# Performance work log

Measured on AMD Instinct MI355X. Metric: run time of the kernel, lower is better.

## Reference

```python
import jax, jax.numpy as jnp
import numpy as np
from jax import lax

C = 173            # EEG channels (independent towers)
L = 400            # samples per channel
POOL_OUT = 10      # AdaptiveMaxPool1d output length (400/10 = 40 exact window)
EPS = 1e-5


def setup_inputs() -> dict:
    key = jax.random.key(0)
    ks = jax.random.split(key, 6)
    B = 64
    x = jax.random.normal(ks[0], (B, C, L), dtype=jnp.float32)
    # per-channel tower 1: Conv1d(1,16,9)  -> grouped kernel [C*16, 1, 9]
    w1 = jax.random.normal(ks[1], (C * 16, 1, 9), dtype=jnp.float32) * 0.2
    b1 = jnp.zeros((C * 16,), jnp.float32)
    g1 = jnp.ones((C * 16,), jnp.float32)
    beta1 = jnp.zeros((C * 16,), jnp.float32)
    m1 = jnp.zeros((C * 16,), jnp.float32)
    v1 = jnp.ones((C * 16,), jnp.float32)
    # per-channel tower 2: Conv1d(16,32,7) -> grouped kernel [C*32, 16, 7]
    w2 = jax.random.normal(ks[2], (C * 32, 16, 7), dtype=jnp.float32) * 0.05
    b2 = jnp.zeros((C * 32,), jnp.float32)
    g2 = jnp.ones((C * 32,), jnp.float32)
    beta2 = jnp.zeros((C * 32,), jnp.float32)
    m2 = jnp.zeros((C * 32,), jnp.float32)
    v2 = jnp.ones((C * 32,), jnp.float32)
    # combiner MLP: Linear(32*C*10, 128) -> ReLU -> Linear(128, 1)
    wc1 = jax.random.normal(ks[3], (128, 32 * C * POOL_OUT), dtype=jnp.float32) * 0.01
    bc1 = jnp.zeros((128,), jnp.float32)
    wc2 = jax.random.normal(ks[4], (1, 128), dtype=jnp.float32) * 0.05
    bc2 = jnp.zeros((1,), jnp.float32)
    return dict(x=x, w1=w1, b1=b1, g1=g1, beta1=beta1, m1=m1, v1=v1,
                w2=w2, b2=b2, g2=g2, beta2=beta2, m2=m2, v2=v2,
                wc1=wc1, bc1=bc1, wc2=wc2, bc2=bc2)


def _bn(y, g, beta, m, v):
    # inference-mode BatchNorm1d over channel axis of [B, CF, L]
    inv = g * lax.rsqrt(v + EPS)
    return y * inv[None, :, None] + (beta - m * inv)[None, :, None]


def reference(x, w1, b1, g1, beta1, m1, v1, w2, b2, g2, beta2, m2, v2, wc1, bc1, wc2, bc2):
    B = x.shape[0]
    dn = ('NCH', 'OIH', 'NCH')
    # tower conv 1: all 173 per-channel Conv1d(1,16,9,pad=4) as one grouped conv
    y = lax.conv_general_dilated(x, w1, (1,), [(4, 4)], dimension_numbers=dn,
                                 feature_group_count=C)           # [B, C*16, 400]
    y = jax.nn.relu(_bn(y + b1[None, :, None], g1, beta1, m1, v1))
    # tower conv 2: Conv1d(16,32,7,pad=3), grouped by channel
    y = lax.conv_general_dilated(y, w2, (1,), [(3, 3)], dimension_numbers=dn,
                                 feature_group_count=C)           # [B, C*32, 400]
    y = jax.nn.relu(_bn(y + b2[None, :, None], g2, beta2, m2, v2))
    # AdaptiveMaxPool1d(10): exact non-overlapping windows of 40
    y = y.reshape(B, C * 32, POOL_OUT, L // POOL_OUT).max(axis=-1)  # [B, C*32, 10]
    # concat of per-channel flattened features == flatten (channel, feat, pos)
    flat = y.reshape(B, C * 32 * POOL_OUT)                          # [B, 55360]
    h = jax.nn.relu(flat @ wc1.T + bc1)
    out = h @ wc2.T + bc2                                           # [B, 1]
    return out
```

## Files before the change

kernel.cpp:

```cpp
#include <hip/hip_runtime.h>

#define C_CH 173
#define L_IN 400
#define EPSV 1e-5f
#define KFEAT 55360

typedef __fp16   fp16x2 __attribute__((ext_vector_type(2)));
typedef _Float16 f16x8  __attribute__((ext_vector_type(8)));
typedef float    f32x4  __attribute__((ext_vector_type(4)));
typedef float    f32x16 __attribute__((ext_vector_type(16)));

#define Y1T_STRIDE_I 9
#define Y1T_ROWS   406

#define SEG_STRIDE 102

#define N1 (173 * 3584)
#define N2 (173 * 512)
#define N3 (173 * 96)

__global__ __launch_bounds__(256) void prep_kernel(
    const float* __restrict__ w1, const float* __restrict__ b1,
    const float* __restrict__ g1, const float* __restrict__ beta1,
    const float* __restrict__ m1, const float* __restrict__ v1,
    const float* __restrict__ w2, const float* __restrict__ b2,
    const float* __restrict__ g2, const float* __restrict__ beta2,
    const float* __restrict__ m2, const float* __restrict__ v2,
    _Float16* __restrict__ w2T_g, _Float16* __restrict__ w1T_g,
    float* __restrict__ sc_g)
{
    const int idx = blockIdx.x * 256 + threadIdx.x;
    if (idx < N1) {
        int c = idx / 3584, r = idx - c * 3584;
        int dt = r >> 9, fg = r & 511;
        int f = fg >> 4, g = fg & 15;
        w2T_g[idx] = (_Float16)w2[c * 3584 + f * 112 + g * 7 + dt];
    } else if (idx < N1 + N2) {
        int j = idx - N1;
        int c = j / 512, r = j - c * 512;
        int g = r >> 5, k = r & 31;
        w1T_g[j] = (k < 9) ? (_Float16)w1[c * 144 + g * 9 + k] : (_Float16)0.0f;
    } else if (idx < N1 + N2 + N3) {
        int j = idx - N1 - N2;
        int c = j / 96, r = j - c * 96;
        float o;
        if (r < 32) {
            int g  = r & 15;
            int cf = c * 16 + g;
            float inv = g1[cf] * rsqrtf(v1[cf] + EPSV);
            o = (r < 16) ? inv : (b1[cf] - m1[cf]) * inv + beta1[cf];
        } else {
            int f  = (r - 32) & 31;
            int cf = c * 32 + f;
            float inv = g2[cf] * rsqrtf(v2[cf] + EPSV);
            o = (r < 64) ? inv : (b2[cf] - m2[cf]) * inv + beta2[cf];
        }
        sc_g[j] = o;
    }
}

__global__ __launch_bounds__(320, 7) void tower_kernel(
    const float* __restrict__ x,
    const _Float16* __restrict__ w2T_g, const _Float16* __restrict__ w1T_g,
    const float* __restrict__ sc_g,
    _Float16* __restrict__ featH)
{
    __shared__ __align__(16) _Float16 xa_s[432];
    __shared__ __align__(16) _Float16 xb_s[432];
    __shared__ __align__(16) _Float16 w1T_s[16 * 32];
    __shared__ __align__(16) _Float16 y1T_s[Y1T_ROWS * 2 * Y1T_STRIDE_I];
    __shared__ __align__(16) _Float16 w2T_s[7 * 512];
    __shared__ _Float16               segmax_s[32 * SEG_STRIDE];
    __shared__ __align__(16) float    cst_s[96];

    const int c   = blockIdx.x;
    const int tid = threadIdx.x;

    {
        const int4* w2src = (const int4*)(w2T_g + (size_t)c * 3584);
        for (int i = tid; i < 448; i += 320) ((int4*)w2T_s)[i] = w2src[i];
        const int4* w1src = (const int4*)(w1T_g + c * 512);
        if (tid < 64) ((int4*)w1T_s)[tid] = w1src[tid];
        const float4* csrc = (const float4*)(sc_g + c * 96);
        if (tid >= 64 && tid < 88) ((float4*)cst_s)[tid - 64] = csrc[tid - 64];
        if (tid >= 88 && tid < 142) {
            int i = tid - 88;
            int r = i / 9, cx = i - r * 9;
            int row = (r < 3) ? r : (400 + r);
            ((int*)y1T_s)[row * Y1T_STRIDE_I + cx] = 0;
        }
    }
    __syncthreads();
    const float s2f  = cst_s[32 + (tid & 31)];
    const float sh2f = cst_s[64 + (tid & 31)];

    const int nlaneH = tid & 31;
    const int halfH  = (tid >> 5) & 1;
    union F8q { int4 q; f16x8 h; } af[7];
#pragma unroll
    for (int dt = 0; dt < 7; ++dt)
        af[dt].q = *(const int4*)((const int*)w2T_s + dt * 256 + nlaneH * 8 + halfH * 4);

    for (int nb = 0; nb < 4; ++nb) {
        const int b = blockIdx.y * 4 + nb;

        const float* xrow = x + ((size_t)b * C_CH + c) * L_IN;
        for (int i = tid; i < 432; i += 320) {
            float v = (i >= 4 && i < 404) ? xrow[i - 4] : 0.0f;
            _Float16 h = (_Float16)v;
            xa_s[i] = h;
            if (i > 0) xb_s[i - 1] = h;
        }
        if (tid == 0) xb_s[431] = (_Float16)0.0f;
        __syncthreads();

        {
            const int lane = tid & 63;
            const int wv5  = tid >> 6;
            const int nl   = lane & 15;
            const int q    = lane >> 4;
            union { int4 v; f16x8 h; } a1;
            a1.v = *(const int4*)((const int*)w1T_s + nl * 16 + q * 4);
            float s1r[4], sh1r[4];
#pragma unroll
            for (int r = 0; r < 4; ++r) {
                s1r[r]  = cst_s[q * 4 + r];
                sh1r[r] = cst_s[16 + q * 4 + r];
            }
            const int* xsel = (const int*)((nl & 1) ? xb_s : xa_s);
            for (int tile = 0; tile < 5; ++tile) {
                const int t0 = (wv5 * 5 + tile) * 16;
                const int dw = (t0 + nl + q * 8) >> 1;
                union { int4 v; f16x8 h; } bf;
                bf.v.x = xsel[dw];
                bf.v.y = xsel[dw + 1];
                bf.v.z = xsel[dw + 2];
                bf.v.w = xsel[dw + 3];
                f32x4 acc = {0.0f, 0.0f, 0.0f, 0.0f};
                acc = __builtin_amdgcn_mfma_f32_16x16x32_f16(a1.h, bf.h, acc, 0, 0, 0);
                union { _Float16 h[4]; int2 d; } pk;
#pragma unroll
                for (int r = 0; r < 4; ++r) {
                    float v = acc[r] * s1r[r] + sh1r[r];
                    pk.h[r] = (_Float16)(v > 0.0f ? v : 0.0f);
                }
                int* yp = (int*)y1T_s + (t0 + nl + 3) * Y1T_STRIDE_I + q * 2;
                yp[0] = pk.d.x;
                yp[1] = pk.d.y;
            }
        }
        __syncthreads();

        {
            const int wv    = tid >> 6;
            const int nlane = nlaneH;
            const int half  = halfH;

            for (int tile = wv; tile < 13; tile += 5) {
                const int tA  = tile * 32 + nlane;
                const int tAr = tA < 400 ? tA : 399;
                f32x16 acc;
#pragma unroll
                for (int i = 0; i < 16; ++i) acc[i] = 0.0f;

#pragma unroll
                for (int dt = 0; dt < 7; ++dt) {
                    const int* p = (const int*)y1T_s + (tAr + dt) * Y1T_STRIDE_I + half * 4;
                    union { int d[4]; f16x8 h; } bf;
                    bf.d[0] = p[0];
                    bf.d[1] = p[1];
                    bf.d[2] = p[2];
                    bf.d[3] = p[3];
                    acc = __builtin_amdgcn_mfma_f32_32x32x16_f16(bf.h, af[dt].h, acc, 0, 0, 0);
                }

                const int base = nlane * SEG_STRIDE + tile * 8 + half;
#pragma unroll
                for (int q = 0; q < 4; ++q) {
                    float v0 = acc[4 * q + 0] * s2f;
                    float v1 = acc[4 * q + 1] * s2f;
                    float v2 = acc[4 * q + 2] * s2f;
                    float v3 = acc[4 * q + 3] * s2f;
                    float m  = fmaxf(fmaxf(v0, v1), fmaxf(v2, v3));
                    const int sub = tile * 8 + 2 * q + half;
                    if (sub < 100) segmax_s[base + 2 * q] = (_Float16)m;
                }
            }
        }
        __syncthreads();

        {
            const int f = tid & 31;
            const int p = tid >> 5;
            float m = -3.0e38f;
#pragma unroll
            for (int k = 0; k < 10; ++k)
                m = fmaxf(m, (float)segmax_s[f * SEG_STRIDE + p * 10 + k]);
            float v = fmaxf(m + sh2f, 0.0f);
            featH[(size_t)b * KFEAT + (c * 32 + f) * 10 + p] = (_Float16)v;
        }
    }
}

__global__ __launch_bounds__(512) void fc1_kernel(
    const _Float16* __restrict__ featH, const float* __restrict__ wc1,
    float* __restrict__ part)
{
    __shared__ float red[4 * 2048];

    const int tid   = threadIdx.x;
    const int kb    = blockIdx.x;
    const int w     = tid >> 6;
    const int lane  = tid & 63;
    const int nlane = lane & 31;
    const int half  = lane >> 5;
    const int kh    = w >> 2;
    const int jq    = w & 3;
    const int jrow  = jq * 32 + nlane;
    const int k0    = kb * 320 + kh * 160;

    const float*    ap  = wc1   + (size_t)jrow * KFEAT + k0 + half * 8;
    const _Float16* b0p = featH + (size_t)nlane * KFEAT + k0 + half * 8;
    const _Float16* b1p = featH + (size_t)(nlane + 32) * KFEAT + k0 + half * 8;

    f32x16 acc0, acc1;
#pragma unroll
    for (int i = 0; i < 16; ++i) { acc0[i] = 0.0f; acc1[i] = 0.0f; }

#pragma unroll 5
    for (int s = 0; s < 10; ++s) {
        const float4 aw0 = *(const float4*)(ap + s * 16);
        const float4 aw1 = *(const float4*)(ap + s * 16 + 4);
        union { fp16x2 v2[4]; f16x8 h; } a;
        a.v2[0] = __builtin_amdgcn_cvt_pkrtz(aw0.x, aw0.y);
        a.v2[1] = __builtin_amdgcn_cvt_pkrtz(aw0.z, aw0.w);
        a.v2[2] = __builtin_amdgcn_cvt_pkrtz(aw1.x, aw1.y);
        a.v2[3] = __builtin_amdgcn_cvt_pkrtz(aw1.z, aw1.w);

        union { int4 q; f16x8 h; } b0, b1;
        b0.q = *(const int4*)(b0p + s * 16);
        b1.q = *(const int4*)(b1p + s * 16);

        acc0 = __builtin_amdgcn_mfma_f32_32x32x16_f16(a.h, b0.h, acc0, 0, 0, 0);
        acc1 = __builtin_amdgcn_mfma_f32_32x32x16_f16(a.h, b1.h, acc1, 0, 0, 0);
    }

    if (kh == 1) {
        float* rp = red + jq * 2048;
#pragma unroll
        for (int reg = 0; reg < 16; ++reg) {
            rp[(reg * 2 + half) * 64 + nlane]      = acc0[reg];
            rp[(reg * 2 + half) * 64 + 32 + nlane] = acc1[reg];
        }
    }
    __syncthreads();
    if (kh == 0) {
        const float* rp = red + jq * 2048;
        float* pt = part + (size_t)kb * 8192;
#pragma unroll
        for (int reg = 0; reg < 16; ++reg) {
            int j = jq * 32 + (reg & 3) + 8 * (reg >> 2) + 4 * half;
            float v0 = acc0[reg] + rp[(reg * 2 + half) * 64 + nlane];
            float v1 = acc1[reg] + rp[(reg * 2 + half) * 64 + 32 + nlane];
            pt[j * 64 + nlane]      = v0;
            pt[j * 64 + 32 + nlane] = v1;
        }
    }
}

__global__ __launch_bounds__(256) void reduce_kernel(
    const float* __restrict__ part, float* __restrict__ h_ws)
{
    const int e = blockIdx.x * 256 + threadIdx.x;
    const float* p = part + e;
    float s0 = 0.0f, s1 = 0.0f, s2 = 0.0f, s3 = 0.0f;
#pragma unroll 4
    for (int kb = 0; kb < 172; kb += 4) {
        s0 += p[(size_t)(kb + 0) * 8192];
        s1 += p[(size_t)(kb + 1) * 8192];
        s2 += p[(size_t)(kb + 2) * 8192];
        s3 += p[(size_t)(kb + 3) * 8192];
    }
    s0 += p[(size_t)172 * 8192];
    h_ws[e] = (s0 + s1) + (s2 + s3);
}

__global__ __launch_bounds__(512) void fc2_kernel(
    const float* __restrict__ h_ws, const float* __restrict__ bc1,
    const float* __restrict__ wc2, const float* __restrict__ bc2,
    float* __restrict__ out)
{
    __shared__ float partial[512];
    const int t  = threadIdx.x;
    const int b  = t & 63;
    const int jc = t >> 6;
    float s = 0.0f;
#pragma unroll
    for (int jj = 0; jj < 16; ++jj) {
        const int j = jc * 16 + jj;
        float hv = h_ws[j * 64 + b] + bc1[j];
        hv = hv > 0.0f ? hv : 0.0f;
        s += wc2[j] * hv;
    }
    partial[t] = s;
    __syncthreads();
    if (t < 64) {
        float r = partial[t];
#pragma unroll
        for (int k = 1; k < 8; ++k) r += partial[t + 64 * k];
        out[b] = r + bc2[0];
    }
}

extern "C" void kernel_launch(void* const* d_in, const int* in_sizes, int n_in,
                              void* d_out, int out_size, void* d_ws, size_t ws_size,
                              hipStream_t stream)
{
    const float* x     = (const float*)d_in[0];
    const float* w1    = (const float*)d_in[1];
    const float* b1    = (const float*)d_in[2];
    const float* g1    = (const float*)d_in[3];
    const float* beta1 = (const float*)d_in[4];
    const float* m1    = (const float*)d_in[5];
    const float* v1    = (const float*)d_in[6];
    const float* w2    = (const float*)d_in[7];
    const float* b2    = (const float*)d_in[8];
    const float* g2    = (const float*)d_in[9];
    const float* beta2 = (const float*)d_in[10];
    const float* m2    = (const float*)d_in[11];
    const float* v2    = (const float*)d_in[12];
    const float* wc1   = (const float*)d_in[13];
    const float* bc1   = (const float*)d_in[14];
    const float* wc2   = (const float*)d_in[15];
    const float* bc2   = (const float*)d_in[16];

    char* ws = (char*)d_ws;
    _Float16* featH = (_Float16*)ws;
    float*    part  = (float*)(ws + 7086080);
    _Float16* w2T_g = (_Float16*)(ws + 12754944);
    _Float16* w1T_g = (_Float16*)(ws + 13995008);
    float*    sc_g  = (float*)(ws + 14172160);
    float*    h_ws  = (float*)(ws + 14238592);

    hipLaunchKernelGGL(prep_kernel, dim3(2834), dim3(256), 0, stream,
                       w1, b1, g1, beta1, m1, v1,
                       w2, b2, g2, beta2, m2, v2, w2T_g, w1T_g, sc_g);

    hipLaunchKernelGGL(tower_kernel, dim3(C_CH, 16), dim3(320), 0, stream,
                       x, w2T_g, w1T_g, sc_g, featH);

    hipLaunchKernelGGL(fc1_kernel, dim3(C_CH), dim3(512), 0, stream,
                       featH, wc1, part);

    hipLaunchKernelGGL(reduce_kernel, dim3(32), dim3(256), 0, stream,
                       part, h_ws);

    hipLaunchKernelGGL(fc2_kernel, dim3(1), dim3(512), 0, stream,
                       h_ws, bc1, wc2, bc2, (float*)d_out);
}
```

Before: 196.8 us.

## Widen tower blocks to seven waves and fuse reduce with fc2 via atomic counter

```diff
diff --git a/kernel.cpp b/kernel.cpp
--- a/kernel.cpp
+++ b/kernel.cpp
@@ -27,7 +27,7 @@
     const float* __restrict__ g2, const float* __restrict__ beta2,
     const float* __restrict__ m2, const float* __restrict__ v2,
     _Float16* __restrict__ w2T_g, _Float16* __restrict__ w1T_g,
-    float* __restrict__ sc_g)
+    float* __restrict__ sc_g, unsigned int* __restrict__ cnt)
 {
     const int idx = blockIdx.x * 256 + threadIdx.x;
     if (idx < N1) {
@@ -56,10 +56,12 @@
             o = (r < 64) ? inv : (b2[cf] - m2[cf]) * inv + beta2[cf];
         }
         sc_g[j] = o;
-    }
-}
-
-__global__ __launch_bounds__(320, 7) void tower_kernel(
+    } else if (idx == N1 + N2 + N3) {
+        cnt[0] = 0u;
+    }
+}
+
+__global__ __launch_bounds__(448, 7) void tower_kernel(
     const float* __restrict__ x,
     const _Float16* __restrict__ w2T_g, const _Float16* __restrict__ w1T_g,
     const float* __restrict__ sc_g,
@@ -78,7 +80,7 @@
 
     {
         const int4* w2src = (const int4*)(w2T_g + (size_t)c * 3584);
-        for (int i = tid; i < 448; i += 320) ((int4*)w2T_s)[i] = w2src[i];
+        ((int4*)w2T_s)[tid] = w2src[tid];
         const int4* w1src = (const int4*)(w1T_g + c * 512);
         if (tid < 64) ((int4*)w1T_s)[tid] = w1src[tid];
         const float4* csrc = (const float4*)(sc_g + c * 96);
@@ -105,18 +107,18 @@
         const int b = blockIdx.y * 4 + nb;
 
         const float* xrow = x + ((size_t)b * C_CH + c) * L_IN;
-        for (int i = tid; i < 432; i += 320) {
-            float v = (i >= 4 && i < 404) ? xrow[i - 4] : 0.0f;
+        if (tid < 432) {
+            float v = (tid >= 4 && tid < 404) ? xrow[tid - 4] : 0.0f;
             _Float16 h = (_Float16)v;
-            xa_s[i] = h;
-            if (i > 0) xb_s[i - 1] = h;
+            xa_s[tid] = h;
+            if (tid > 0) xb_s[tid - 1] = h;
         }
         if (tid == 0) xb_s[431] = (_Float16)0.0f;
         __syncthreads();
 
         {
             const int lane = tid & 63;
-            const int wv5  = tid >> 6;
+            const int wv7  = tid >> 6;
             const int nl   = lane & 15;
             const int q    = lane >> 4;
             union { int4 v; f16x8 h; } a1;
@@ -128,8 +130,8 @@
                 sh1r[r] = cst_s[16 + q * 4 + r];
             }
             const int* xsel = (const int*)((nl & 1) ? xb_s : xa_s);
-            for (int tile = 0; tile < 5; ++tile) {
-                const int t0 = (wv5 * 5 + tile) * 16;
+            for (int tile = wv7; tile < 25; tile += 7) {
+                const int t0 = tile * 16;
                 const int dw = (t0 + nl + q * 8) >> 1;
                 union { int4 v; f16x8 h; } bf;
                 bf.v.x = xsel[dw];
@@ -152,11 +154,11 @@
         __syncthreads();
 
         {
-            const int wv    = tid >> 6;
+            const int wv7   = tid >> 6;
             const int nlane = nlaneH;
             const int half  = halfH;
 
-            for (int tile = wv; tile < 13; tile += 5) {
+            for (int tile = wv7; tile < 13; tile += 7) {
                 const int tA  = tile * 32 + nlane;
                 const int tAr = tA < 400 ? tA : 399;
                 f32x16 acc;
@@ -189,7 +191,7 @@
         }
         __syncthreads();
 
-        {
+        if (tid < 320) {
             const int f = tid & 31;
             const int p = tid >> 5;
             float m = -3.0e38f;
@@ -268,47 +270,61 @@
     }
 }
 
-__global__ __launch_bounds__(256) void reduce_kernel(
-    const float* __restrict__ part, float* __restrict__ h_ws)
-{
-    const int e = blockIdx.x * 256 + threadIdx.x;
-    const float* p = part + e;
+__global__ __launch_bounds__(256) void reduce_fc2_kernel(
+    const float* __restrict__ part, const float* __restrict__ bc1,
+    const float* __restrict__ wc2, const float* __restrict__ bc2,
+    float* __restrict__ h_ws, unsigned int* __restrict__ cnt,
+    float* __restrict__ out)
+{
+    __shared__ float buf[256];
+    __shared__ unsigned int isLast;
+
+    const int m = blockIdx.x;
+    const int t = threadIdx.x;
+    const int e = m * 128 + (t & 127);
+    const int kk = t >> 7;
+    const int n  = kk ? 85 : 88;
+    const float* p = part + (size_t)(kk ? 88 : 0) * 8192 + e;
+
     float s0 = 0.0f, s1 = 0.0f, s2 = 0.0f, s3 = 0.0f;
-#pragma unroll 4
-    for (int kb = 0; kb < 172; kb += 4) {
+    int kb = 0;
+    for (; kb + 4 <= n; kb += 4) {
         s0 += p[(size_t)(kb + 0) * 8192];
         s1 += p[(size_t)(kb + 1) * 8192];
         s2 += p[(size_t)(kb + 2) * 8192];
         s3 += p[(size_t)(kb + 3) * 8192];
     }
-    s0 += p[(size_t)172 * 8192];
-    h_ws[e] = (s0 + s1) + (s2 + s3);
-}
-
-__global__ __launch_bounds__(512) void fc2_kernel(
-    const float* __restrict__ h_ws, const float* __restrict__ bc1,
-    const float* __restrict__ wc2, const float* __restrict__ bc2,
-    float* __restrict__ out)
-{
-    __shared__ float partial[512];
-    const int t  = threadIdx.x;
-    const int b  = t & 63;
-    const int jc = t >> 6;
-    float s = 0.0f;
-#pragma unroll
-    for (int jj = 0; jj < 16; ++jj) {
-        const int j = jc * 16 + jj;
-        float hv = h_ws[j * 64 + b] + bc1[j];
-        hv = hv > 0.0f ? hv : 0.0f;
-        s += wc2[j] * hv;
-    }
-    partial[t] = s;
-    __syncthreads();
-    if (t < 64) {
-        float r = partial[t];
-#pragma unroll
-        for (int k = 1; k < 8; ++k) r += partial[t + 64 * k];
-        out[b] = r + bc2[0];
+    for (; kb < n; ++kb) s0 += p[(size_t)kb * 8192];
+    buf[t] = (s0 + s1) + (s2 + s3);
+    __syncthreads();
+    if (t < 128) h_ws[e] = buf[t] + buf[t + 128];
+
+    __syncthreads();
+    if (t == 0) {
+        __threadfence();
+        unsigned int old = __hip_atomic_fetch_add(
+            cnt, 1u, __ATOMIC_ACQ_REL, __HIP_MEMORY_SCOPE_AGENT);
+        isLast = (old == 63u) ? 1u : 0u;
+    }
+    __syncthreads();
+    if (isLast) {
+        __threadfence();
+        const int b  = t & 63;
+        const int jc = t >> 6;
+        float s = 0.0f;
+#pragma unroll
+        for (int jj = 0; jj < 32; ++jj) {
+            const int j = jc * 32 + jj;
+            float hv = __hip_atomic_load(&h_ws[j * 64 + b],
+                                         __ATOMIC_RELAXED,
+                                         __HIP_MEMORY_SCOPE_AGENT) + bc1[j];
+            hv = hv > 0.0f ? hv : 0.0f;
+            s += wc2[j] * hv;
+        }
+        buf[t] = s;
+        __syncthreads();
+        if (t < 64)
+            out[t] = buf[t] + buf[t + 64] + buf[t + 128] + buf[t + 192] + bc2[0];
     }
 }
 
@@ -335,26 +351,24 @@
     const float* bc2   = (const float*)d_in[16];
 
     char* ws = (char*)d_ws;
-    _Float16* featH = (_Float16*)ws;
-    float*    part  = (float*)(ws + 7086080);
-    _Float16* w2T_g = (_Float16*)(ws + 12754944);
-    _Float16* w1T_g = (_Float16*)(ws + 13995008);
-    float*    sc_g  = (float*)(ws + 14172160);
-    float*    h_ws  = (float*)(ws + 14238592);
+    _Float16*     featH = (_Float16*)ws;
+    float*        part  = (float*)(ws + 7086080);
+    _Float16*     w2T_g = (_Float16*)(ws + 12754944);
+    _Float16*     w1T_g = (_Float16*)(ws + 13995008);
+    float*        sc_g  = (float*)(ws + 14172160);
+    float*        h_ws  = (float*)(ws + 14238592);
+    unsigned int* cnt   = (unsigned int*)(ws + 14271360);
 
     hipLaunchKernelGGL(prep_kernel, dim3(2834), dim3(256), 0, stream,
                        w1, b1, g1, beta1, m1, v1,
-                       w2, b2, g2, beta2, m2, v2, w2T_g, w1T_g, sc_g);
-
-    hipLaunchKernelGGL(tower_kernel, dim3(C_CH, 16), dim3(320), 0, stream,
+                       w2, b2, g2, beta2, m2, v2, w2T_g, w1T_g, sc_g, cnt);
+
+    hipLaunchKernelGGL(tower_kernel, dim3(C_CH, 16), dim3(448), 0, stream,
                        x, w2T_g, w1T_g, sc_g, featH);
 
     hipLaunchKernelGGL(fc1_kernel, dim3(C_CH), dim3(512), 0, stream,
                        featH, wc1, part);
 
-    hipLaunchKernelGGL(reduce_kernel, dim3(32), dim3(256), 0, stream,
-                       part, h_ws);
-
-    hipLaunchKernelGGL(fc2_kernel, dim3(1), dim3(512), 0, stream,
-                       h_ws, bc1, wc2, bc2, (float*)d_out);
-}
+    hipLaunchKernelGGL(reduce_fc2_kernel, dim3(64), dim3(256), 0, stream,
+                       part, bc1, wc2, bc2, h_ws, cnt, (float*)d_out);
+}
```

New measurement: 183.4 us. 6.8% less time.
